# Kernel optimization log

Hardware: AMD Instinct MI355X
Metric: run time of the kernel (lower is better)

## Reference

```python
import jax, jax.numpy as jnp
import numpy as np

B, C, T, H, W = 4, 256, 64, 32, 32
K = 64  # kernel_size spans the whole sequence


def setup_inputs() -> dict:
    key = jax.random.key(0)
    kx, kw = jax.random.split(key)
    x = jax.random.normal(kx, (B, C, T, H, W), dtype=jnp.float32)
    # nn.Parameter(torch.randn(channels, 1, kernel_size) * 0.01)
    weight = jax.random.normal(kw, (C, 1, K), dtype=jnp.float32) * 0.01
    return {"x": x, "weight": weight}


def reference(x, weight):
    b, c, t, h, w = x.shape
    k = weight.shape[-1]
    pad = k - 1
    # torch .view: raw row-major reinterpretation of (B,C,T,H,W) as (B*H*W, C, T)
    x_ = x.reshape(b * h * w, c, t)
    # depthwise (groups=C) cross-correlation, symmetric padding like F.conv1d(padding=pad)
    y = jax.lax.conv_general_dilated(
        x_, weight,
        window_strides=(1,),
        padding=[(pad, pad)],
        feature_group_count=c,
        dimension_numbers=("NCH", "OIH", "NCH"),
    )  # (B*H*W, C, T + pad)
    y = y[:, :, -t:]  # causal slice: keep last T positions
    # .view(B,H,W,C,T).permute(0,3,4,1,2) -> (B,C,T,H,W)
    y = y.reshape(b, h, w, c, t).transpose(0, 3, 4, 1, 2)
    return y
```

## Files before the change

kernel.cpp:

```cpp
#include <hip/hip_runtime.h>


constexpr int Cc = 256;
constexpr int Tt = 64;
constexpr int Kk = 64;
constexpr int CT = Cc * Tt;

__global__ __launch_bounds__(256, 3)
void DepthwiseTemporalConv_24962349924982_kernel(const float* __restrict__ x,
                                                 const float* __restrict__ w,
                                                 float* __restrict__ out) {
    const int tid  = threadIdx.x;
    const int lane = tid & 63;
    const int wv   = tid >> 6;

    const int n_tile = blockIdx.x & 63;
    const int c_tile = blockIdx.x >> 6;
    const int n  = n_tile * 64 + lane;
    const int cv = c_tile * 4 + wv;

    const int cu = __builtin_amdgcn_readfirstlane(cv);
    const float* __restrict__ wp = w + (size_t)cu * Kk;
    float wr[Kk];
    #pragma unroll
    for (int m = 0; m < 16; ++m) {
        const float4 v = *(const float4*)(wp + 4 * m);
        wr[4*m+0] = v.x; wr[4*m+1] = v.y; wr[4*m+2] = v.z; wr[4*m+3] = v.w;
    }

    float acc[Tt];
    #pragma unroll
    for (int t = 0; t < Tt; ++t) acc[t] = 0.f;

    const float4* __restrict__ rp =
        (const float4*)(x + (size_t)n * CT + (size_t)cu * Tt);
    #pragma unroll
    for (int m = 0; m < 16; ++m) {
        const float4 v = rp[m];
        const float e[4] = {v.x, v.y, v.z, v.w};
        #pragma unroll
        for (int q = 0; q < 4; ++q) {
            const int j = 4 * m + q;
            const float xv = e[q];
            #pragma unroll
            for (int t = 0; t <= j; ++t)
                acc[t] = fmaf(xv, wr[j - t], acc[t]);
        }
    }

    float* __restrict__ obase = out + (size_t)(n >> 10) * (Cc * Tt * 1024)
                                    + (size_t)cv * (Tt * 1024) + (n & 1023);
    #pragma unroll
    for (int t = 0; t < Tt; ++t)
        obase[(size_t)t * 1024] = acc[t];
}

extern "C" void kernel_launch(void* const* d_in, const int* in_sizes, int n_in,
                              void* d_out, int out_size, void* d_ws, size_t ws_size,
                              hipStream_t stream) {
    const float* x = (const float*)d_in[0];
    const float* w = (const float*)d_in[1];
    float* out = (float*)d_out;
    DepthwiseTemporalConv_24962349924982_kernel<<<dim3(4096), dim3(256), 0, stream>>>(x, w, out);
}
```

Baseline: 152.6 us.

## Stage input through LDS via async global_load_lds in two halves, split accumulators

Measured after the change: 149.7 us. About the same (-1.9%).

```diff
diff --git a/kernel.cpp b/kernel.cpp
--- a/kernel.cpp
+++ b/kernel.cpp
@@ -5,54 +5,125 @@
 constexpr int Tt = 64;
 constexpr int Kk = 64;
 constexpr int CT = Cc * Tt;
+constexpr int CS = 1024 + 16;
+constexpr int WAVE_LDS = 8 * CS;
+constexpr int LDS_BYTES = 4 * WAVE_LDS;
 
-__global__ __launch_bounds__(256, 3)
+__global__ __launch_bounds__(256, 4)
 void DepthwiseTemporalConv_24962349924982_kernel(const float* __restrict__ x,
                                                  const float* __restrict__ w,
                                                  float* __restrict__ out) {
+    __shared__ __align__(16) char lds[LDS_BYTES];
     const int tid  = threadIdx.x;
     const int lane = tid & 63;
     const int wv   = tid >> 6;
 
     const int n_tile = blockIdx.x & 63;
     const int c_tile = blockIdx.x >> 6;
-    const int n  = n_tile * 64 + lane;
-    const int cv = c_tile * 4 + wv;
+    const int n0 = n_tile * 64;
+    const int n  = n0 + lane;
+    const int cu = __builtin_amdgcn_readfirstlane(c_tile * 4 + wv);
 
-    const int cu = __builtin_amdgcn_readfirstlane(cv);
-    const float* __restrict__ wp = w + (size_t)cu * Kk;
-    float wr[Kk];
+    char* wbase = lds + wv * WAVE_LDS;
+    const int srow = lane >> 3;
+    const int scol = (lane & 7) * 4;
+
     #pragma unroll
-    for (int m = 0; m < 16; ++m) {
-        const float4 v = *(const float4*)(wp + 4 * m);
-        wr[4*m+0] = v.x; wr[4*m+1] = v.y; wr[4*m+2] = v.z; wr[4*m+3] = v.w;
+    for (int i = 0; i < 8; ++i) {
+        const float* gsrc = x + (size_t)(n0 + 8 * i + srow) * CT
+                              + (size_t)cu * Tt + scol;
+        __builtin_amdgcn_global_load_lds(
+            (const __attribute__((address_space(1))) void*)gsrc,
+            (__attribute__((address_space(3))) void*)(wbase + i * CS),
+            16, 0, 0);
     }
 
-    float acc[Tt];
-    #pragma unroll
-    for (int t = 0; t < Tt; ++t) acc[t] = 0.f;
-
-    const float4* __restrict__ rp =
-        (const float4*)(x + (size_t)n * CT + (size_t)cu * Tt);
-    #pragma unroll
-    for (int m = 0; m < 16; ++m) {
-        const float4 v = rp[m];
-        const float e[4] = {v.x, v.y, v.z, v.w};
+    float wr[Kk];
+    {
+        const float4* wp = (const float4*)(w + (size_t)cu * Kk);
         #pragma unroll
-        for (int q = 0; q < 4; ++q) {
-            const int j = 4 * m + q;
-            const float xv = e[q];
-            #pragma unroll
-            for (int t = 0; t <= j; ++t)
-                acc[t] = fmaf(xv, wr[j - t], acc[t]);
+        for (int m = 0; m < 16; ++m) {
+            const float4 v = wp[m];
+            wr[4*m+0] = v.x; wr[4*m+1] = v.y; wr[4*m+2] = v.z; wr[4*m+3] = v.w;
         }
     }
 
+    asm volatile("s_waitcnt vmcnt(0)" ::: "memory");
+    __builtin_amdgcn_sched_barrier(0);
+
+    const char* rbase = wbase + (lane >> 3) * CS + (lane & 7) * 128;
+    float xh[32];
+    #pragma unroll
+    for (int m = 0; m < 8; ++m) {
+        const float4 v = *(const float4*)(rbase + m * 16);
+        xh[4*m+0] = v.x; xh[4*m+1] = v.y; xh[4*m+2] = v.z; xh[4*m+3] = v.w;
+    }
+    asm volatile("s_waitcnt lgkmcnt(0)" ::: "memory");
+    __builtin_amdgcn_sched_barrier(0);
+    #pragma unroll
+    for (int m = 0; m < 8; ++m)
+        asm volatile("" : "+v"(xh[4*m+0]), "+v"(xh[4*m+1]),
+                          "+v"(xh[4*m+2]), "+v"(xh[4*m+3]));
+
+    #pragma unroll
+    for (int i = 0; i < 8; ++i) {
+        const float* gsrc = x + (size_t)(n0 + 8 * i + srow) * CT
+                              + (size_t)cu * Tt + 32 + scol;
+        __builtin_amdgcn_global_load_lds(
+            (const __attribute__((address_space(1))) void*)gsrc,
+            (__attribute__((address_space(3))) void*)(wbase + i * CS),
+            16, 0, 0);
+    }
+    __builtin_amdgcn_sched_barrier(0);
+
+    float acc[32];
+    #pragma unroll
+    for (int t = 0; t < 32; ++t) acc[t] = 0.f;
+    #pragma unroll
+    for (int j = 0; j < 32; ++j) {
+        const float xv = xh[j];
+        #pragma unroll
+        for (int t = 0; t <= j; ++t)
+            acc[t] = fmaf(xv, wr[j - t], acc[t]);
+    }
+
+    asm volatile("s_waitcnt vmcnt(0)" ::: "memory");
+    __builtin_amdgcn_sched_barrier(0);
+
+    float xh2[32];
+    #pragma unroll
+    for (int m = 0; m < 8; ++m) {
+        const float4 v = *(const float4*)(rbase + m * 16);
+        xh2[4*m+0] = v.x; xh2[4*m+1] = v.y; xh2[4*m+2] = v.z; xh2[4*m+3] = v.w;
+    }
+
+    #pragma unroll
+    for (int j = 0; j < 32; ++j) {
+        const float xv = xh2[j];
+        #pragma unroll
+        for (int t = 0; t < 32; ++t)
+            acc[t] = fmaf(xv, wr[32 + j - t], acc[t]);
+    }
+
     float* __restrict__ obase = out + (size_t)(n >> 10) * (Cc * Tt * 1024)
-                                    + (size_t)cv * (Tt * 1024) + (n & 1023);
+                                    + (size_t)cu * (Tt * 1024) + (n & 1023);
     #pragma unroll
-    for (int t = 0; t < Tt; ++t)
+    for (int t = 0; t < 32; ++t)
         obase[(size_t)t * 1024] = acc[t];
+
+    float acc2[32];
+    #pragma unroll
+    for (int t = 0; t < 32; ++t) acc2[t] = 0.f;
+    #pragma unroll
+    for (int j = 0; j < 32; ++j) {
+        const float xv = xh2[j];
+        #pragma unroll
+        for (int t = 0; t <= j; ++t)
+            acc2[t] = fmaf(xv, wr[j - t], acc2[t]);
+    }
+    #pragma unroll
+    for (int t = 0; t < 32; ++t)
+        obase[(size_t)(32 + t) * 1024] = acc2[t];
 }
 
 extern "C" void kernel_launch(void* const* d_in, const int* in_sizes, int n_in,
```
